# Kernel optimization log

Hardware: AMD Instinct MI355X
Metric: run time of the kernel (lower is better)

The kernel has to match this reference:

```python
import jax, jax.numpy as jnp
import numpy as np
import math

VOCAB = 32000
D = 128           # embedding_size
S = 4096          # max_seq_len
B = 4
N_W = math.ceil(math.log2(S))   # 12
K = N_W + 1                      # n_links = 13


def _chord_cols():
    # col[i, 0] = i ; col[i, k] = (i + 2**(k-1)) % S  for k = 1..K-1
    i = np.arange(S)[:, None]
    offs = np.concatenate([[0], 2 ** np.arange(K - 1)])
    return jnp.asarray((i + offs[None, :]) % S, dtype=jnp.int32)


def setup_inputs() -> dict:
    key = jax.random.key(0)
    ks = jax.random.split(key, 8)
    sc = 0.02
    return {
        "data": jax.random.randint(ks[0], (B, S), 0, VOCAB),
        "cols": _chord_cols(),
        "emb": jax.random.normal(ks[1], (VOCAB, D), jnp.float32) * sc,
        "apc": jax.random.normal(ks[2], (S, D), jnp.float32) * sc,
        "g_W1": jax.random.normal(ks[3], (D, D), jnp.float32) * sc,
        "g_b1": jnp.zeros((D,), jnp.float32),
        "g_W2": jax.random.normal(ks[4], (D, D), jnp.float32) * sc,
        "g_b2": jnp.zeros((D,), jnp.float32),
        "f_W1": jax.random.normal(ks[5], (N_W, D, D), jnp.float32) * sc,
        "f_b1": jnp.zeros((N_W, D), jnp.float32),
        "f_W2": jax.random.normal(ks[6], (N_W, D, K), jnp.float32) * sc,
        "f_b2": jnp.zeros((N_W, K), jnp.float32),
    }


def reference(data, cols, emb, apc, g_W1, g_b1, g_W2, g_b2, f_W1, f_b1, f_W2, f_b2):
    # token + absolute position embeddings (dropouts are identity in eval)
    x = emb[data] + apc[None, :, :]                       # [B, S, D]
    # V = g(x): Linear -> GELU -> Linear
    V = jax.nn.gelu(x @ g_W1 + g_b1, approximate=False) @ g_W2 + g_b2  # [B, S, D]
    res = V
    # Precompute all n_W per-position mixing weight tensors W_m = f_m(x)
    h = jax.nn.gelu(jnp.einsum('bsd,mde->mbse', x, f_W1) + f_b1[:, None, None, :],
                    approximate=False)                    # [M, B, S, D]
    W_all = jnp.einsum('mbse,mek->mbsk', h, f_W2) + f_b2[:, None, None, :]  # [M, B, S, K]

    def step(V, W_m):
        # chord spmm: out[b,i,:] = sum_k W_m[b,i,k] * V[b, cols[i,k], :]
        V = jnp.einsum('bsk,bskd->bsd', W_m, V[:, cols, :]) + res
        return V, None

    V, _ = jax.lax.scan(step, V, W_all)
    return V
```

## Files before the change

### kernel.cpp

```cpp
#include <hip/hip_runtime.h>
#include <hip/hip_bf16.h>

typedef __bf16 bf16x8 __attribute__((ext_vector_type(8)));
typedef float  f32x4  __attribute__((ext_vector_type(4)));
typedef unsigned short u16x8 __attribute__((ext_vector_type(8)));

#define NTOK 16384
#define SEQ  4096
#define DIM  128
#define NSEG 13
#define NM   12
#define NK   13

__device__ inline unsigned short f2bf(float f) {
    unsigned int u = __float_as_uint(f);
    unsigned int r = (u + 0x7FFFu + ((u >> 16) & 1u)) >> 16;
    return (unsigned short)r;
}
__device__ inline float bf2f(unsigned short h) {
    return __uint_as_float(((unsigned int)h) << 16);
}
__device__ inline float uaf(unsigned int u) { return __uint_as_float(u); }
__device__ inline unsigned int cvtpk(float a, float b) {
    unsigned int r;
    asm("v_cvt_pk_bf16_f32 %0, %1, %2" : "=v"(r) : "v"(a), "v"(b));
    return r;
}

__device__ inline float gelu_f(float u) {
    const float c0 = 0.3989422804f;
    const float c1 = -0.0664903801f;
    const float c2 = 0.0099735570f;
    float u2 = u * u;
    float p  = __builtin_fmaf(u2, c2, c1);
    p        = __builtin_fmaf(u2, p, c0);
    return __builtin_fmaf(u2, p, 0.5f * u);
}

__device__ inline int swz(int u16idx) {
    int byte = u16idx << 1;
    byte ^= ((byte >> 8) & 7) << 4;
    return byte >> 1;
}

#define EMB_BLOCKS 8192
#define CONV_BLOCKS ((NSEG * DIM * DIM + 255) / 256)
__global__ __launch_bounds__(256) void prep_kernel(
    const int* __restrict__ data, const float* __restrict__ emb,
    const float* __restrict__ apc, unsigned short* __restrict__ xb,
    const float* __restrict__ g_W1, const float* __restrict__ g_W2,
    const float* __restrict__ f_W1, const float* __restrict__ f_W2,
    unsigned short* __restrict__ wb1T, unsigned short* __restrict__ wb2Tg,
    unsigned short* __restrict__ wb2Tf)
{
    int tid = threadIdx.x;
    if (blockIdx.x < EMB_BLOCKS) {
        int n = blockIdx.x * 2 + (tid >> 7);
        int d = tid & 127;
        int s = n & (SEQ - 1);
        int tok = data[n];
        float v = emb[(size_t)tok * DIM + d] + apc[s * DIM + d];
        xb[(size_t)n * DIM + d] = f2bf(v);
    } else {
        int i = (blockIdx.x - EMB_BLOCKS) * 256 + tid;
        if (i < NSEG * DIM * DIM) {
            int seg = i >> 14;
            int e = (i >> 7) & 127;
            int d = i & 127;
            float v = (seg == 0) ? g_W1[d * DIM + e]
                                 : f_W1[((seg - 1) * DIM + d) * DIM + e];
            wb1T[i] = f2bf(v);
        }
        if (i < DIM * DIM) {
            int c = i >> 7, e = i & 127;
            wb2Tg[i] = f2bf(g_W2[e * DIM + c]);
        }
        if (i < NM * 16 * DIM) {
            int m = i >> 11;
            int c = (i >> 7) & 15;
            int e = i & 127;
            float v = (c < NK) ? f_W2[(m * DIM + e) * NK + c] : 0.f;
            wb2Tf[i] = f2bf(v);
        }
    }
}

__global__ __launch_bounds__(256, 3) void mlp_kernel(
    const unsigned short* __restrict__ xb,
    const unsigned short* __restrict__ wb1T,
    const unsigned short* __restrict__ wb2Tg,
    const unsigned short* __restrict__ wb2Tf,
    const float* __restrict__ g_b1, const float* __restrict__ g_b2,
    const float* __restrict__ f_b1, const float* __restrict__ f_b2,
    float* __restrict__ resF, unsigned short* __restrict__ resB,
    unsigned short* __restrict__ Wallb)
{
    const int seg  = blockIdx.y;
    const int row0 = blockIdx.x * 64;
    const int tid  = threadIdx.x;
    const int wave = tid >> 6;
    const int lane = tid & 63;

    __shared__ __align__(16) unsigned short Hs[4][16 * DIM];
    __shared__ __align__(16) unsigned short W1s[DIM * DIM];
    __shared__ __align__(16) unsigned short W2fs[16 * DIM];

    const int r16   = lane & 15;
    const int kgrp  = (lane >> 4) * 8;
    const int crow0 = (lane >> 4) << 2;

    const float* b1p = (seg == 0) ? g_b1 : (f_b1 + (seg - 1) * DIM);
    float bias1[8];
    #pragma unroll
    for (int t = 0; t < 8; ++t) bias1[t] = b1p[t * 16 + r16];
    float bias2[8];
    float bias2f = 0.f;
    if (seg == 0) {
        #pragma unroll
        for (int t = 0; t < 8; ++t) bias2[t] = g_b2[t * 16 + r16];
    } else {
        bias2f = (r16 < NK) ? f_b2[(seg - 1) * NK + r16] : 0.f;
    }

    {
        const int4* wg = reinterpret_cast<const int4*>(wb1T + (size_t)seg * DIM * DIM);
        #pragma unroll
        for (int i = 0; i < 8; ++i)
            *reinterpret_cast<int4*>(&W1s[swz((tid + i * 256) * 8)]) = wg[tid + i * 256];
    }
    if (seg != 0) {
        const int4* wg = reinterpret_cast<const int4*>(wb2Tf + (size_t)(seg - 1) * 16 * DIM);
        *reinterpret_cast<int4*>(&W2fs[swz(tid * 8)]) = wg[tid];
    }
    __syncthreads();

    const unsigned short* xrow = xb + (size_t)(row0 + wave * 16 + r16) * DIM + kgrp;
    f32x4 acc[8];
    #pragma unroll
    for (int t = 0; t < 8; ++t) acc[t] = (f32x4){0.f, 0.f, 0.f, 0.f};
    #pragma unroll
    for (int kk = 0; kk < 4; ++kk) {
        bf16x8 a = *reinterpret_cast<const bf16x8*>(xrow + kk * 32);
        #pragma unroll
        for (int t = 0; t < 8; ++t) {
            bf16x8 b = *reinterpret_cast<const bf16x8*>(&W1s[swz((t * 16 + r16) * DIM + kk * 32 + kgrp)]);
            acc[t] = __builtin_amdgcn_mfma_f32_16x16x32_bf16(a, b, acc[t], 0, 0, 0);
        }
    }

    unsigned short* hs = Hs[wave];
    #pragma unroll
    for (int t = 0; t < 8; ++t) {
        int col = t * 16 + r16;
        #pragma unroll
        for (int r = 0; r < 4; r += 2) {
            float g0 = gelu_f(acc[t][r]     + bias1[t]);
            float g1 = gelu_f(acc[t][r + 1] + bias1[t]);
            unsigned int pk = cvtpk(g0, g1);
            hs[swz((crow0 + r)     * DIM + col)] = (unsigned short)pk;
            hs[swz((crow0 + r + 1) * DIM + col)] = (unsigned short)(pk >> 16);
        }
    }

    if (seg == 0) {
        f32x4 acc2[8];
        #pragma unroll
        for (int t = 0; t < 8; ++t) acc2[t] = (f32x4){0.f, 0.f, 0.f, 0.f};
        #pragma unroll
        for (int kk = 0; kk < 4; ++kk) {
            bf16x8 a = *reinterpret_cast<const bf16x8*>(&hs[swz(r16 * DIM + kk * 32 + kgrp)]);
            #pragma unroll
            for (int t = 0; t < 8; ++t) {
                bf16x8 b = *reinterpret_cast<const bf16x8*>(wb2Tg + (size_t)(t * 16 + r16) * DIM + kk * 32 + kgrp);
                acc2[t] = __builtin_amdgcn_mfma_f32_16x16x32_bf16(a, b, acc2[t], 0, 0, 0);
            }
        }
        #pragma unroll
        for (int t = 0; t < 8; ++t) {
            int col = t * 16 + r16;
            #pragma unroll
            for (int r = 0; r < 4; r += 2) {
                int grow = row0 + wave * 16 + crow0 + r;
                float v0 = acc2[t][r]     + bias2[t];
                float v1 = acc2[t][r + 1] + bias2[t];
                resF[(size_t)grow * DIM + col]       = v0;
                resF[(size_t)(grow + 1) * DIM + col] = v1;
                unsigned int pk = cvtpk(v0, v1);
                resB[(size_t)grow * DIM + col]       = (unsigned short)pk;
                resB[(size_t)(grow + 1) * DIM + col] = (unsigned short)(pk >> 16);
            }
        }
    } else {
        int m = seg - 1;
        f32x4 acc2 = (f32x4){0.f, 0.f, 0.f, 0.f};
        #pragma unroll
        for (int kk = 0; kk < 4; ++kk) {
            bf16x8 a = *reinterpret_cast<const bf16x8*>(&hs[swz(r16 * DIM + kk * 32 + kgrp)]);
            bf16x8 b = *reinterpret_cast<const bf16x8*>(&W2fs[swz(r16 * DIM + kk * 32 + kgrp)]);
            acc2 = __builtin_amdgcn_mfma_f32_16x16x32_bf16(a, b, acc2, 0, 0, 0);
        }
        #pragma unroll
        for (int r = 0; r < 4; r += 2) {
            int grow = row0 + wave * 16 + crow0 + r;
            unsigned int pk = cvtpk(acc2[r] + bias2f, acc2[r + 1] + bias2f);
            Wallb[((size_t)m * NTOK + grow) * 16 + r16]     = (unsigned short)pk;
            Wallb[((size_t)m * NTOK + grow + 1) * 16 + r16] = (unsigned short)(pk >> 16);
        }
    }
}

#define CCH 2
#define RPAD 512
#define PADTOK (SEQ + RPAD)
__global__ __launch_bounds__(1024) void scan_lds_kernel(
    const unsigned short* __restrict__ resB,
    const float* __restrict__ resF,
    const unsigned short* __restrict__ Wallb,
    float* __restrict__ outF)
{
    __shared__ unsigned int V32[2 * PADTOK];

    const int bid = (int)blockIdx.x;
    const int bb    = (bid >> 1) & 3;
    const int chunk = ((bid >> 3) << 1) | (bid & 1);
    const int d0  = chunk * CCH;
    const int tid = threadIdx.x;

    unsigned int resP[4];
    unsigned int Bv[4];
    #pragma unroll
    for (int j = 0; j < 4; ++j) {
        int t = j * 1024 + tid;
        int n = (bb << 12) + t;
        unsigned int r = *reinterpret_cast<const unsigned int*>(resB + (size_t)n * DIM + d0);
        resP[j] = r;
        Bv[j] = r;
        V32[t] = r;
    }
    if (tid < RPAD) V32[SEQ + tid] = Bv[0];

    const unsigned short* wb0 = Wallb + (size_t)(bb << 12) * 16;
    __syncthreads();

    unsigned int curbase = 0;

    #pragma unroll 1
    for (int m = 0; m < NM - 1; ++m) {
        uint4 wA[4][2];
        {
            const unsigned short* wp = wb0 + (size_t)m * NTOK * 16;
            #pragma unroll
            for (int j = 0; j < 4; ++j) {
                const uint4* wrow = reinterpret_cast<const uint4*>(wp + (size_t)(j * 1024 + tid) * 16);
                wA[j][0] = wrow[0]; wA[j][1] = wrow[1];
            }
        }

        unsigned int vt[4][10];
        #pragma unroll
        for (int q = 0; q < 10; ++q) {
            #pragma unroll
            for (int j = 0; j < 4; ++j)
                vt[j][q] = V32[curbase + j * 1024 + tid + (1 << q)];
        }
        __builtin_amdgcn_sched_barrier(0);

        const unsigned int nb = curbase ^ PADTOK;
        float o0[4], o1[4];
        #pragma unroll
        for (int j = 0; j < 4; ++j) {
            o0[j] = uaf(resP[j] << 16);
            o1[j] = uaf(resP[j] & 0xffff0000u);
        }

        #pragma unroll
        for (int k = 0; k < NK; ++k) {
            #pragma unroll
            for (int j = 0; j < 4; ++j) {
                uint4 wa = wA[j][0], wbv = wA[j][1];
                unsigned int ww =
                    (k < 2) ? wa.x : (k < 4) ? wa.y : (k < 6) ? wa.z : (k < 8) ? wa.w :
                    (k < 10) ? wbv.x : (k < 12) ? wbv.y : wbv.z;
                float w = (k & 1) ? uaf(ww & 0xffff0000u) : uaf(ww << 16);
                unsigned int v;
                if (k == 0)       v = Bv[j];
                else if (k == 11) v = Bv[(j + 1) & 3];
                else if (k == 12) v = Bv[(j + 2) & 3];
                else              v = vt[j][k - 1];
                o0[j] = __builtin_fmaf(w, uaf(v << 16),          o0[j]);
                o1[j] = __builtin_fmaf(w, uaf(v & 0xffff0000u), o1[j]);
            }
        }

        #pragma unroll
        for (int j = 0; j < 4; ++j) {
            unsigned int pk = cvtpk(o0[j], o1[j]);
            Bv[j] = pk;
            V32[nb + j * 1024 + tid] = pk;
        }
        if (tid < RPAD) V32[nb + SEQ + tid] = Bv[0];

        __syncthreads();
        curbase = nb;
    }

    {
        float2 rfv[4];
        #pragma unroll
        for (int j = 0; j < 4; ++j) {
            int n = (bb << 12) + j * 1024 + tid;
            rfv[j] = *reinterpret_cast<const float2*>(resF + (size_t)n * DIM + d0);
        }
        uint4 wA[4][2];
        {
            const unsigned short* wp = wb0 + (size_t)(NM - 1) * NTOK * 16;
            #pragma unroll
            for (int j = 0; j < 4; ++j) {
                const uint4* wrow = reinterpret_cast<const uint4*>(wp + (size_t)(j * 1024 + tid) * 16);
                wA[j][0] = wrow[0]; wA[j][1] = wrow[1];
            }
        }

        unsigned int vt[4][10];
        #pragma unroll
        for (int q = 0; q < 10; ++q) {
            #pragma unroll
            for (int j = 0; j < 4; ++j)
                vt[j][q] = V32[curbase + j * 1024 + tid + (1 << q)];
        }
        __builtin_amdgcn_sched_barrier(0);

        float o0[4], o1[4];
        #pragma unroll
        for (int j = 0; j < 4; ++j) { o0[j] = rfv[j].x; o1[j] = rfv[j].y; }

        #pragma unroll
        for (int k = 0; k < NK; ++k) {
            #pragma unroll
            for (int j = 0; j < 4; ++j) {
                uint4 wa = wA[j][0], wbv = wA[j][1];
                unsigned int ww =
                    (k < 2) ? wa.x : (k < 4) ? wa.y : (k < 6) ? wa.z : (k < 8) ? wa.w :
                    (k < 10) ? wbv.x : (k < 12) ? wbv.y : wbv.z;
                float w = (k & 1) ? uaf(ww & 0xffff0000u) : uaf(ww << 16);
                unsigned int v;
                if (k == 0)       v = Bv[j];
                else if (k == 11) v = Bv[(j + 1) & 3];
                else if (k == 12) v = Bv[(j + 2) & 3];
                else              v = vt[j][k - 1];
                o0[j] = __builtin_fmaf(w, uaf(v << 16),          o0[j]);
                o1[j] = __builtin_fmaf(w, uaf(v & 0xffff0000u), o1[j]);
            }
        }

        #pragma unroll
        for (int j = 0; j < 4; ++j) {
            int n = (bb << 12) + j * 1024 + tid;
            float2 o; o.x = o0[j]; o.y = o1[j];
            *reinterpret_cast<float2*>(outF + (size_t)n * DIM + d0) = o;
        }
    }
}

extern "C" void kernel_launch(void* const* d_in, const int* in_sizes, int n_in,
                              void* d_out, int out_size, void* d_ws, size_t ws_size,
                              hipStream_t stream) {
    const int*   data = (const int*)  d_in[0];
    const float* emb  = (const float*)d_in[2];
    const float* apc  = (const float*)d_in[3];
    const float* g_W1 = (const float*)d_in[4];
    const float* g_b1 = (const float*)d_in[5];
    const float* g_W2 = (const float*)d_in[6];
    const float* g_b2 = (const float*)d_in[7];
    const float* f_W1 = (const float*)d_in[8];
    const float* f_b1 = (const float*)d_in[9];
    const float* f_W2 = (const float*)d_in[10];
    const float* f_b2 = (const float*)d_in[11];
    float* out = (float*)d_out;

    char* ws = (char*)d_ws;
    size_t off = 0;
    auto alloc = [&](size_t bytes) {
        void* p = ws + off;
        off += (bytes + 255) & ~(size_t)255;
        return p;
    };
    unsigned short* xb    = (unsigned short*)alloc((size_t)NTOK * DIM * 2);
    unsigned short* wb1T  = (unsigned short*)alloc((size_t)NSEG * DIM * DIM * 2);
    unsigned short* wb2Tg = (unsigned short*)alloc((size_t)DIM * DIM * 2);
    unsigned short* wb2Tf = (unsigned short*)alloc((size_t)NM * 16 * DIM * 2);
    float*          resF  = (float*)alloc((size_t)NTOK * DIM * 4);
    unsigned short* resB  = (unsigned short*)alloc((size_t)NTOK * DIM * 2);
    unsigned short* Wallb = (unsigned short*)alloc((size_t)NM * NTOK * 16 * 2);
    (void)ws_size; (void)in_sizes; (void)n_in; (void)out_size;

    prep_kernel<<<EMB_BLOCKS + CONV_BLOCKS, 256, 0, stream>>>(
        data, emb, apc, xb, g_W1, g_W2, f_W1, f_W2, wb1T, wb2Tg, wb2Tf);

    dim3 grid(NTOK / 64, NSEG);
    mlp_kernel<<<grid, 256, 0, stream>>>(xb, wb1T, wb2Tg, wb2Tf,
                                         g_b1, g_b2, f_b1, f_b2, resF, resB, Wallb);

    scan_lds_kernel<<<256, 1024, 0, stream>>>(resB, resF, Wallb, out);
}
```

Baseline: 74.27 us.

## Scan one dimension per block and pack two sequence halves per LDS word

The scan kernel now gives each block a single feature dimension instead of two, so it launches 512 blocks of 512 threads rather than 256 blocks of 1024. Each 32-bit LDS word packs the values of token t and token t+2048, which halves the LDS footprint and lets each thread cover two sequence positions per word. The wrap-around for the long chord offsets is handled with register half-swaps and a swapped pad region. The aim is more parallelism and lower LDS use per block. In exchange, weight rows are loaded twice per step and resF/outF accesses become scalar and strided.

```diff
diff --git a/kernel.cpp b/kernel.cpp
--- a/kernel.cpp
+++ b/kernel.cpp
@@ -209,155 +209,207 @@
     }
 }
 
-#define CCH 2
-#define RPAD 512
-#define PADTOK (SEQ + RPAD)
-__global__ __launch_bounds__(1024) void scan_lds_kernel(
+#define NW 2048
+#define PADW 512
+#define WTOT (NW + PADW)
+__global__ __launch_bounds__(512) void scan_lds_kernel(
     const unsigned short* __restrict__ resB,
     const float* __restrict__ resF,
     const unsigned short* __restrict__ Wallb,
     float* __restrict__ outF)
 {
-    __shared__ unsigned int V32[2 * PADTOK];
+    __shared__ unsigned int V32[2 * WTOT];
 
     const int bid = (int)blockIdx.x;
-    const int bb    = (bid >> 1) & 3;
-    const int chunk = ((bid >> 3) << 1) | (bid & 1);
-    const int d0  = chunk * CCH;
+    const int bb  = (bid >> 1) & 3;
+    const int d0  = ((bid >> 3) << 1) | (bid & 1);
     const int tid = threadIdx.x;
 
-    unsigned int resP[4];
-    unsigned int Bv[4];
-    #pragma unroll
-    for (int j = 0; j < 4; ++j) {
-        int t = j * 1024 + tid;
-        int n = (bb << 12) + t;
-        unsigned int r = *reinterpret_cast<const unsigned int*>(resB + (size_t)n * DIM + d0);
-        resP[j] = r;
-        Bv[j] = r;
-        V32[t] = r;
-    }
-    if (tid < RPAD) V32[SEQ + tid] = Bv[0];
-
+    unsigned int resW[4];
+    unsigned int Bw[4];
+    {
+        unsigned int rlo[8];
+        #pragma unroll
+        for (int jj = 0; jj < 8; ++jj) {
+            int n = (bb << 12) + jj * 512 + tid;
+            rlo[jj] = (unsigned int)resB[(size_t)n * DIM + d0];
+        }
+        #pragma unroll
+        for (int jj = 0; jj < 4; ++jj) {
+            unsigned int w = rlo[jj] | (rlo[jj + 4] << 16);
+            resW[jj] = w;
+            Bw[jj]   = w;
+            V32[jj * 512 + tid] = w;
+        }
+        V32[NW + tid] = (Bw[0] >> 16) | (Bw[0] << 16);
+    }
     const unsigned short* wb0 = Wallb + (size_t)(bb << 12) * 16;
     __syncthreads();
 
-    unsigned int curbase = 0;
+    unsigned int cur = 0;
 
     #pragma unroll 1
     for (int m = 0; m < NM - 1; ++m) {
-        uint4 wA[4][2];
-        {
-            const unsigned short* wp = wb0 + (size_t)m * NTOK * 16;
-            #pragma unroll
-            for (int j = 0; j < 4; ++j) {
-                const uint4* wrow = reinterpret_cast<const uint4*>(wp + (size_t)(j * 1024 + tid) * 16);
-                wA[j][0] = wrow[0]; wA[j][1] = wrow[1];
-            }
-        }
+        const unsigned short* wp = wb0 + (size_t)m * NTOK * 16;
 
         unsigned int vt[4][10];
         #pragma unroll
         for (int q = 0; q < 10; ++q) {
             #pragma unroll
-            for (int j = 0; j < 4; ++j)
-                vt[j][q] = V32[curbase + j * 1024 + tid + (1 << q)];
+            for (int jj = 0; jj < 4; ++jj)
+                vt[jj][q] = V32[cur + jj * 512 + tid + (1 << q)];
+        }
+        unsigned int wA[4][7];
+        #pragma unroll
+        for (int jj = 0; jj < 4; ++jj) {
+            const unsigned int* wr = reinterpret_cast<const unsigned int*>(wp + (size_t)(jj * 512 + tid) * 16);
+            uint4 a = *reinterpret_cast<const uint4*>(wr);
+            uint2 b = *reinterpret_cast<const uint2*>(wr + 4);
+            wA[jj][0] = a.x; wA[jj][1] = a.y; wA[jj][2] = a.z; wA[jj][3] = a.w;
+            wA[jj][4] = b.x; wA[jj][5] = b.y; wA[jj][6] = wr[6];
         }
         __builtin_amdgcn_sched_barrier(0);
 
-        const unsigned int nb = curbase ^ PADTOK;
-        float o0[4], o1[4];
-        #pragma unroll
-        for (int j = 0; j < 4; ++j) {
-            o0[j] = uaf(resP[j] << 16);
-            o1[j] = uaf(resP[j] & 0xffff0000u);
-        }
-
+        float oA[4];
+        #pragma unroll
+        for (int jj = 0; jj < 4; ++jj) oA[jj] = uaf(resW[jj] << 16);
         #pragma unroll
         for (int k = 0; k < NK; ++k) {
             #pragma unroll
-            for (int j = 0; j < 4; ++j) {
-                uint4 wa = wA[j][0], wbv = wA[j][1];
-                unsigned int ww =
-                    (k < 2) ? wa.x : (k < 4) ? wa.y : (k < 6) ? wa.z : (k < 8) ? wa.w :
-                    (k < 10) ? wbv.x : (k < 12) ? wbv.y : wbv.z;
+            for (int jj = 0; jj < 4; ++jj) {
+                unsigned int ww = wA[jj][k >> 1];
                 float w = (k & 1) ? uaf(ww & 0xffff0000u) : uaf(ww << 16);
-                unsigned int v;
-                if (k == 0)       v = Bv[j];
-                else if (k == 11) v = Bv[(j + 1) & 3];
-                else if (k == 12) v = Bv[(j + 2) & 3];
-                else              v = vt[j][k - 1];
-                o0[j] = __builtin_fmaf(w, uaf(v << 16),          o0[j]);
-                o1[j] = __builtin_fmaf(w, uaf(v & 0xffff0000u), o1[j]);
-            }
-        }
-
-        #pragma unroll
-        for (int j = 0; j < 4; ++j) {
-            unsigned int pk = cvtpk(o0[j], o1[j]);
-            Bv[j] = pk;
-            V32[nb + j * 1024 + tid] = pk;
-        }
-        if (tid < RPAD) V32[nb + SEQ + tid] = Bv[0];
-
+                unsigned int vbits;
+                if (k == 0)       vbits = Bw[jj] << 16;
+                else if (k == 11) vbits = (jj < 2) ? (Bw[jj + 2] << 16) : (Bw[jj - 2] & 0xffff0000u);
+                else if (k == 12) vbits = Bw[jj] & 0xffff0000u;
+                else              vbits = vt[jj][k - 1] << 16;
+                oA[jj] = __builtin_fmaf(w, uaf(vbits), oA[jj]);
+            }
+        }
+
+        unsigned int wB[4][7];
+        #pragma unroll
+        for (int jj = 0; jj < 4; ++jj) {
+            const unsigned int* wr = reinterpret_cast<const unsigned int*>(wp + (size_t)(NW + jj * 512 + tid) * 16);
+            uint4 a = *reinterpret_cast<const uint4*>(wr);
+            uint2 b = *reinterpret_cast<const uint2*>(wr + 4);
+            wB[jj][0] = a.x; wB[jj][1] = a.y; wB[jj][2] = a.z; wB[jj][3] = a.w;
+            wB[jj][4] = b.x; wB[jj][5] = b.y; wB[jj][6] = wr[6];
+        }
+
+        float oB[4];
+        #pragma unroll
+        for (int jj = 0; jj < 4; ++jj) oB[jj] = uaf(resW[jj] & 0xffff0000u);
+        #pragma unroll
+        for (int k = 0; k < NK; ++k) {
+            #pragma unroll
+            for (int jj = 0; jj < 4; ++jj) {
+                unsigned int ww = wB[jj][k >> 1];
+                float w = (k & 1) ? uaf(ww & 0xffff0000u) : uaf(ww << 16);
+                unsigned int vbits;
+                if (k == 0)       vbits = Bw[jj] & 0xffff0000u;
+                else if (k == 11) vbits = (jj < 2) ? (Bw[jj + 2] & 0xffff0000u) : (Bw[jj - 2] << 16);
+                else if (k == 12) vbits = Bw[jj] << 16;
+                else              vbits = vt[jj][k - 1] & 0xffff0000u;
+                oB[jj] = __builtin_fmaf(w, uaf(vbits), oB[jj]);
+            }
+        }
+
+        const unsigned int nxt = cur ^ WTOT;
+        unsigned int w0 = 0;
+        #pragma unroll
+        for (int jj = 0; jj < 4; ++jj) {
+            unsigned int w = cvtpk(oA[jj], oB[jj]);
+            Bw[jj] = w;
+            V32[nxt + jj * 512 + tid] = w;
+            if (jj == 0) w0 = w;
+        }
+        V32[nxt + NW + tid] = (w0 >> 16) | (w0 << 16);
         __syncthreads();
-        curbase = nb;
+        cur = nxt;
     }
 
     {
-        float2 rfv[4];
-        #pragma unroll
-        for (int j = 0; j < 4; ++j) {
-            int n = (bb << 12) + j * 1024 + tid;
-            rfv[j] = *reinterpret_cast<const float2*>(resF + (size_t)n * DIM + d0);
-        }
-        uint4 wA[4][2];
-        {
-            const unsigned short* wp = wb0 + (size_t)(NM - 1) * NTOK * 16;
-            #pragma unroll
-            for (int j = 0; j < 4; ++j) {
-                const uint4* wrow = reinterpret_cast<const uint4*>(wp + (size_t)(j * 1024 + tid) * 16);
-                wA[j][0] = wrow[0]; wA[j][1] = wrow[1];
-            }
-        }
+        const unsigned short* wp = wb0 + (size_t)(NM - 1) * NTOK * 16;
 
         unsigned int vt[4][10];
         #pragma unroll
         for (int q = 0; q < 10; ++q) {
             #pragma unroll
-            for (int j = 0; j < 4; ++j)
-                vt[j][q] = V32[curbase + j * 1024 + tid + (1 << q)];
+            for (int jj = 0; jj < 4; ++jj)
+                vt[jj][q] = V32[cur + jj * 512 + tid + (1 << q)];
+        }
+        unsigned int wA[4][7];
+        #pragma unroll
+        for (int jj = 0; jj < 4; ++jj) {
+            const unsigned int* wr = reinterpret_cast<const unsigned int*>(wp + (size_t)(jj * 512 + tid) * 16);
+            uint4 a = *reinterpret_cast<const uint4*>(wr);
+            uint2 b = *reinterpret_cast<const uint2*>(wr + 4);
+            wA[jj][0] = a.x; wA[jj][1] = a.y; wA[jj][2] = a.z; wA[jj][3] = a.w;
+            wA[jj][4] = b.x; wA[jj][5] = b.y; wA[jj][6] = wr[6];
         }
         __builtin_amdgcn_sched_barrier(0);
 
-        float o0[4], o1[4];
-        #pragma unroll
-        for (int j = 0; j < 4; ++j) { o0[j] = rfv[j].x; o1[j] = rfv[j].y; }
-
+        float oA[4];
+        #pragma unroll
+        for (int jj = 0; jj < 4; ++jj) {
+            int n = (bb << 12) + jj * 512 + tid;
+            oA[jj] = resF[(size_t)n * DIM + d0];
+        }
         #pragma unroll
         for (int k = 0; k < NK; ++k) {
             #pragma unroll
-            for (int j = 0; j < 4; ++j) {
-                uint4 wa = wA[j][0], wbv = wA[j][1];
-                unsigned int ww =
-                    (k < 2) ? wa.x : (k < 4) ? wa.y : (k < 6) ? wa.z : (k < 8) ? wa.w :
-                    (k < 10) ? wbv.x : (k < 12) ? wbv.y : wbv.z;
+            for (int jj = 0; jj < 4; ++jj) {
+                unsigned int ww = wA[jj][k >> 1];
                 float w = (k & 1) ? uaf(ww & 0xffff0000u) : uaf(ww << 16);
-                unsigned int v;
-                if (k == 0)       v = Bv[j];
-                else if (k == 11) v = Bv[(j + 1) & 3];
-                else if (k == 12) v = Bv[(j + 2) & 3];
-                else              v = vt[j][k - 1];
-                o0[j] = __builtin_fmaf(w, uaf(v << 16),          o0[j]);
-                o1[j] = __builtin_fmaf(w, uaf(v & 0xffff0000u), o1[j]);
-            }
-        }
-
-        #pragma unroll
-        for (int j = 0; j < 4; ++j) {
-            int n = (bb << 12) + j * 1024 + tid;
-            float2 o; o.x = o0[j]; o.y = o1[j];
-            *reinterpret_cast<float2*>(outF + (size_t)n * DIM + d0) = o;
+                unsigned int vbits;
+                if (k == 0)       vbits = Bw[jj] << 16;
+                else if (k == 11) vbits = (jj < 2) ? (Bw[jj + 2] << 16) : (Bw[jj - 2] & 0xffff0000u);
+                else if (k == 12) vbits = Bw[jj] & 0xffff0000u;
+                else              vbits = vt[jj][k - 1] << 16;
+                oA[jj] = __builtin_fmaf(w, uaf(vbits), oA[jj]);
+            }
+        }
+        #pragma unroll
+        for (int jj = 0; jj < 4; ++jj) {
+            int n = (bb << 12) + jj * 512 + tid;
+            outF[(size_t)n * DIM + d0] = oA[jj];
+        }
+
+        unsigned int wB[4][7];
+        #pragma unroll
+        for (int jj = 0; jj < 4; ++jj) {
+            const unsigned int* wr = reinterpret_cast<const unsigned int*>(wp + (size_t)(NW + jj * 512 + tid) * 16);
+            uint4 a = *reinterpret_cast<const uint4*>(wr);
+            uint2 b = *reinterpret_cast<const uint2*>(wr + 4);
+            wB[jj][0] = a.x; wB[jj][1] = a.y; wB[jj][2] = a.z; wB[jj][3] = a.w;
+            wB[jj][4] = b.x; wB[jj][5] = b.y; wB[jj][6] = wr[6];
+        }
+        float oB[4];
+        #pragma unroll
+        for (int jj = 0; jj < 4; ++jj) {
+            int n = (bb << 12) + NW + jj * 512 + tid;
+            oB[jj] = resF[(size_t)n * DIM + d0];
+        }
+        #pragma unroll
+        for (int k = 0; k < NK; ++k) {
+            #pragma unroll
+            for (int jj = 0; jj < 4; ++jj) {
+                unsigned int ww = wB[jj][k >> 1];
+                float w = (k & 1) ? uaf(ww & 0xffff0000u) : uaf(ww << 16);
+                unsigned int vbits;
+                if (k == 0)       vbits = Bw[jj] & 0xffff0000u;
+                else if (k == 11) vbits = (jj < 2) ? (Bw[jj + 2] & 0xffff0000u) : (Bw[jj - 2] << 16);
+                else if (k == 12) vbits = Bw[jj] << 16;
+                else              vbits = vt[jj][k - 1] & 0xffff0000u;
+                oB[jj] = __builtin_fmaf(w, uaf(vbits), oB[jj]);
+            }
+        }
+        #pragma unroll
+        for (int jj = 0; jj < 4; ++jj) {
+            int n = (bb << 12) + NW + jj * 512 + tid;
+            outF[(size_t)n * DIM + d0] = oB[jj];
         }
     }
 }
@@ -401,5 +453,5 @@
     mlp_kernel<<<grid, 256, 0, stream>>>(xb, wb1T, wb2Tg, wb2Tf,
                                          g_b1, g_b2, f_b1, f_b2, resF, resB, Wallb);
 
-    scan_lds_kernel<<<256, 1024, 0, stream>>>(resB, resF, Wallb, out);
-}
+    scan_lds_kernel<<<512, 512, 0, stream>>>(resB, resF, Wallb, out);
+}
```

Result: slower. 93.02 us (+25.2%).
